# Optimization experiments

Hardware: AMD Instinct MI355X
Metric: run time of the kernel (lower is better)

The kernel has to match this reference:

```python
import jax, jax.numpy as jnp
import numpy as np

N, F, D, K = 4096, 128, 64, 2  # nodes, in_dim, out_dim, hops


def setup_inputs() -> dict:
    key = jax.random.key(0)
    k_x, k_a, k_e, k_w = jax.random.split(key, 4)
    X = jax.random.normal(k_x, (N, F), jnp.float32)
    # K+1 non-negative dense adjacency/distance matrices (stacked list)
    A = jax.random.uniform(k_a, (K + 1, N, N), jnp.float32)
    # Dense(out_dim, use_bias=False) weights, glorot-like scale
    W_emb = jax.random.normal(k_e, (F, D), jnp.float32) / np.sqrt(F)
    W_hops = jax.random.normal(k_w, (K + 1, F, D), jnp.float32) / np.sqrt(F)
    alpha = jnp.float32(0.1)
    return {"X": X, "A": A, "W_emb": W_emb, "W_hops": W_hops, "alpha": alpha}


def reference(X, A, W_emb, W_hops, alpha):
    # learned embeddings E = Dense(X)  -> [N, D]
    E = X @ W_emb
    # shared low-rank update alpha * E @ E^T  -> [N, N]
    low_rank = alpha * (E @ E.T)
    # per-hop kernel projections Dense_k(X)  -> [K+1, N, D]
    XW = jnp.einsum('nf,kfd->knd', X, W_hops)
    out = jnp.zeros((N, D), X.dtype)
    for k in range(A.shape[0]):  # fixed small K+1 hops
        A_hat = A[k] + low_rank                       # [N, N]
        deg = jnp.sum(A_hat, axis=1)                  # row sums
        d = jnp.power(deg, -0.5)                      # D^{-1/2}
        # D^{-1/2} A_hat D^{-1/2} via broadcast scaling (same math as diag matmuls)
        A_norm = d[:, None] * A_hat * d[None, :]
        out = out + A_norm @ XW[k]
    return jax.nn.relu(out)
```

## Files before the change

kernel.cpp:

```cpp
#include <hip/hip_runtime.h>
#include <math.h>

#define N_ 4096
#define F_ 128
#define D_ 64
#define KH_ 3
#define ZS_ 16
#define KC_ (N_ / ZS_)
#define BM_ 256

#define OFF_E      0
#define OFF_XW     (N_*D_)
#define OFF_SE     (OFF_XW + KH_*N_*D_)
#define OFF_T      (OFF_SE + D_)
#define OFF_DVEC   (OFF_T + KH_*D_*D_)
#define OFF_YT     (OFF_DVEC + KH_*N_)
#define OFF_AYP    (OFF_YT + KH_*D_*N_/2)
#define OFF_ABF    (OFF_AYP + ZS_*KH_*N_*D_)

typedef __attribute__((ext_vector_type(8))) short bf16x8;
typedef __attribute__((ext_vector_type(4))) float f32x4;

static __device__ __forceinline__ unsigned short f2bf(float f) {
  union { float f; unsigned u; } v; v.f = f;
  unsigned r = (v.u + 0x7fffu + ((v.u >> 16) & 1u)) >> 16;
  return (unsigned short)r;
}

static __device__ __forceinline__ void gload_lds16(const unsigned short* g,
                                                   unsigned short* l) {
  __builtin_amdgcn_global_load_lds(
      (__attribute__((address_space(1))) unsigned int*)g,
      (__attribute__((address_space(3))) unsigned int*)l, 16, 0, 0);
}

__global__ __launch_bounds__(256) void proj_kernel(
    const float* __restrict__ X, const float* __restrict__ W_emb,
    const float* __restrict__ W_hops, float* __restrict__ ws)
{
  __shared__ __align__(16) float sXT[32][68];
  __shared__ __align__(16) float sW[32][68];
  const int t = threadIdx.x;
  const int m = blockIdx.y;
  const int row0 = blockIdx.x * 64;
  const float* W = (m == 0) ? W_emb : (W_hops + (size_t)(m - 1) * F_ * D_);
  float* out = (m == 0) ? (ws + OFF_E) : (ws + OFF_XW + (size_t)(m - 1) * N_ * D_);
  const int tx = t & 15, ty = t >> 4;
  const int d0 = tx * 4, i0 = ty * 4;
  float acc[4][4] = {};
  for (int fc = 0; fc < F_; fc += 32) {
    {
      int i_l = t >> 3;
      int f_l = (t & 7) * 4;
      for (int r = 0; r < 2; ++r) {
        int i = i_l + r * 32;
        float4 v = *(const float4*)(X + (size_t)(row0 + i) * F_ + fc + f_l);
        sXT[f_l + 0][i] = v.x; sXT[f_l + 1][i] = v.y;
        sXT[f_l + 2][i] = v.z; sXT[f_l + 3][i] = v.w;
      }
      int f2 = t >> 4;
      int d  = (t & 15) * 4;
      for (int r = 0; r < 2; ++r) {
        int f = f2 + r * 16;
        *(float4*)&sW[f][d] = *(const float4*)(W + (size_t)(fc + f) * D_ + d);
      }
    }
    __syncthreads();
#pragma unroll 8
    for (int f = 0; f < 32; ++f) {
      float a[4], b[4];
      *(float4*)a = *(const float4*)&sXT[f][i0];
      *(float4*)b = *(const float4*)&sW[f][d0];
      for (int x = 0; x < 4; ++x)
        for (int y = 0; y < 4; ++y)
          acc[x][y] += a[x] * b[y];
    }
    __syncthreads();
  }
  for (int x = 0; x < 4; ++x)
    *(float4*)(out + (size_t)(row0 + i0 + x) * D_ + d0) = *(float4*)acc[x];
  if (m == 0) {
    float p[4];
    for (int y = 0; y < 4; ++y)
      p[y] = acc[0][y] + acc[1][y] + acc[2][y] + acc[3][y];
    *(float4*)&sXT[ty][d0] = *(float4*)p;
    __syncthreads();
    if (ty < 4) {
      int c = ty * 16 + tx;
      float s = 0.f;
#pragma unroll
      for (int r = 0; r < 16; ++r) s += sXT[r][c];
      atomicAdd(ws + OFF_SE + c, s);
    }
  }
}

__global__ __launch_bounds__(256) void degconv_kernel(
    const float* __restrict__ A, const float* __restrict__ E,
    const float* __restrict__ S, const float* __restrict__ alpha_p,
    float* __restrict__ dvec, unsigned short* __restrict__ Abf)
{
  int lane = threadIdx.x & 63;
  int wave = threadIdx.x >> 6;
  int row = blockIdx.x * 4 + wave;
  int i = row & (N_ - 1);
  const float4* Ar = (const float4*)(A + (size_t)row * N_);
  unsigned short* Br = Abf + (size_t)row * N_;
  float s = 0.f;
#pragma unroll
  for (int it = 0; it < 8; ++it) {
    float4 v0 = Ar[it * 128 + lane * 2 + 0];
    float4 v1 = Ar[it * 128 + lane * 2 + 1];
    s += (v0.x + v0.y) + (v0.z + v0.w) + (v1.x + v1.y) + (v1.z + v1.w);
    union { unsigned short u[8]; uint4 q; } pk;
    pk.u[0] = f2bf(v0.x); pk.u[1] = f2bf(v0.y);
    pk.u[2] = f2bf(v0.z); pk.u[3] = f2bf(v0.w);
    pk.u[4] = f2bf(v1.x); pk.u[5] = f2bf(v1.y);
    pk.u[6] = f2bf(v1.z); pk.u[7] = f2bf(v1.w);
    *(uint4*)(Br + (size_t)it * 512 + lane * 8) = pk.q;
  }
  float alpha = *alpha_p;
  s += alpha * E[(size_t)i * D_ + lane] * S[lane];
#pragma unroll
  for (int off = 32; off > 0; off >>= 1)
    s += __shfl_xor(s, off);
  if (lane == 0) dvec[row] = 1.0f / sqrtf(s);
}

__global__ __launch_bounds__(256) void prep_kernel(float* __restrict__ ws,
                                                   float* __restrict__ T)
{
  const int k = blockIdx.y;
  const float* XWk = ws + OFF_XW + (size_t)k * N_ * D_;
  const float* dk  = ws + OFF_DVEC + (size_t)k * N_;
  int t = threadIdx.x;

  if (blockIdx.x < 64) {
    const int j0 = blockIdx.x * 64;
    unsigned short* Ytk = (unsigned short*)(ws + OFF_YT) + (size_t)k * D_ * N_;
    __shared__ float sT[64][65];
    {
      int j = t >> 2;
      int c0 = (t & 3) * 16;
      float dv = dk[j0 + j];
      for (int r = 0; r < 4; ++r) {
        float4 v = *(const float4*)(XWk + (size_t)(j0 + j) * D_ + c0 + 4 * r);
        sT[c0 + 4 * r + 0][j] = v.x * dv;
        sT[c0 + 4 * r + 1][j] = v.y * dv;
        sT[c0 + 4 * r + 2][j] = v.z * dv;
        sT[c0 + 4 * r + 3][j] = v.w * dv;
      }
    }
    __syncthreads();
    {
      int n = t >> 2;
      int jq = (t & 3) * 16;
      __align__(16) unsigned short buf[16];
#pragma unroll
      for (int i = 0; i < 16; ++i) buf[i] = f2bf(sT[n][jq + i]);
      uint4* dst = (uint4*)(Ytk + (size_t)n * N_ + j0 + jq);
      dst[0] = *(uint4*)&buf[0];
      dst[1] = *(uint4*)&buf[8];
    }
  } else {
    const float* E = ws + OFF_E;
    __shared__ __align__(16) float sE[32][68];
    __shared__ __align__(16) float sY[32][68];
    int tx = t & 15, ty = t >> 4;
    int d0 = tx * 4, c0 = ty * 4;
    float acc[4][4] = {};
    int base0 = (blockIdx.x - 64) * 128;
    for (int sub = 0; sub < 4; ++sub) {
      int base = base0 + sub * 32;
      {
        int i_l = t >> 3;
        int c   = (t & 7) * 4;
        float dv = dk[base + i_l];
        for (int r = 0; r < 2; ++r) {
          int col = c + r * 32;
          *(float4*)&sE[i_l][col] = *(const float4*)(E + (size_t)(base + i_l) * D_ + col);
          float4 y = *(const float4*)(XWk + (size_t)(base + i_l) * D_ + col);
          y.x *= dv; y.y *= dv; y.z *= dv; y.w *= dv;
          *(float4*)&sY[i_l][col] = y;
        }
      }
      __syncthreads();
#pragma unroll 8
      for (int i = 0; i < 32; ++i) {
        float c4[4], y4[4];
        *(float4*)c4 = *(const float4*)&sE[i][c0];
        *(float4*)y4 = *(const float4*)&sY[i][d0];
        for (int a = 0; a < 4; ++a)
          for (int b = 0; b < 4; ++b)
            acc[a][b] += c4[a] * y4[b];
      }
      __syncthreads();
    }
    float* Tk = T + (size_t)k * D_ * D_;
    for (int a = 0; a < 4; ++a)
      for (int b = 0; b < 4; ++b)
        atomicAdd(&Tk[(c0 + a) * D_ + d0 + b], acc[a][b]);
  }
}

__global__ __launch_bounds__(256, 3) void agemm_kernel(
    const float* __restrict__ ws, float* __restrict__ AYp)
{
  const int k = blockIdx.y;
  const int row0 = blockIdx.x * BM_;
  const int kz0 = blockIdx.z * KC_;
  const unsigned short* Ak = (const unsigned short*)(ws + OFF_ABF) + ((size_t)k << 24);
  const unsigned short* Ytk = (const unsigned short*)(ws + OFF_YT) + (size_t)k * D_ * N_;

  __shared__ __align__(16) unsigned short sA[BM_ * 64];
  __shared__ __align__(16) unsigned short sY[64 * 64];

  const int t = threadIdx.x;
  const int lane = t & 63;
  const int w = t >> 6;
  const int m = lane & 15;
  const int q = lane >> 4;
  const int sr = t >> 3;
  const int sc = t & 7;

  f32x4 acc[4][4];
#pragma unroll
  for (int a = 0; a < 4; ++a)
#pragma unroll
    for (int b = 0; b < 4; ++b) acc[a][b] = (f32x4){0.f, 0.f, 0.f, 0.f};

  for (int kt = 0; kt < KC_; kt += 64) {
#pragma unroll
    for (int j = 0; j < 8; ++j) {
      int r = j * 32 + sr;
      gload_lds16(Ak + (size_t)(row0 + r) * N_ + (kz0 + kt) + ((sc ^ (r & 7)) << 3),
                  &sA[j * 2048 + t * 8]);
    }
#pragma unroll
    for (int j = 0; j < 2; ++j) {
      int r = j * 32 + sr;
      gload_lds16(Ytk + (size_t)r * N_ + (kz0 + kt) + ((sc ^ (r & 7)) << 3),
                  &sY[j * 2048 + t * 8]);
    }
    __syncthreads();
#pragma unroll
    for (int s = 0; s < 2; ++s) {
      bf16x8 av[4], bv[4];
#pragma unroll
      for (int mr = 0; mr < 4; ++mr) {
        int row = w * 64 + mr * 16 + m;
        av[mr] = *(const bf16x8*)&sA[row * 64 + (((s * 4 + q) ^ (row & 7)) << 3)];
      }
#pragma unroll
      for (int nt = 0; nt < 4; ++nt) {
        int n = nt * 16 + m;
        bv[nt] = *(const bf16x8*)&sY[n * 64 + (((s * 4 + q) ^ (n & 7)) << 3)];
      }
#pragma unroll
      for (int mr = 0; mr < 4; ++mr)
#pragma unroll
        for (int nt = 0; nt < 4; ++nt)
          acc[mr][nt] = __builtin_amdgcn_mfma_f32_16x16x32_bf16(av[mr], bv[nt],
                                                                acc[mr][nt], 0, 0, 0);
    }
    __syncthreads();
  }
#pragma unroll
  for (int mr = 0; mr < 4; ++mr) {
    float* outp = AYp + (((size_t)blockIdx.z * KH_ + k) * N_ + row0 + w * 64 + mr * 16) * D_;
#pragma unroll
    for (int nt = 0; nt < 4; ++nt)
#pragma unroll
      for (int r = 0; r < 4; ++r)
        outp[(size_t)(q * 4 + r) * D_ + nt * 16 + m] = acc[mr][nt][r];
  }
}

__global__ __launch_bounds__(256) void epilogue_kernel(
    const float* __restrict__ ws, const float* __restrict__ alpha_p,
    float* __restrict__ out)
{
  int g = blockIdx.x * 256 + threadIdx.x;
  int i = g >> 6, d = g & 63;
  const float* E    = ws + OFF_E;
  const float* T    = ws + OFF_T;
  const float* dvec = ws + OFF_DVEC;
  const float* AYp  = ws + OFF_AYP;
  float alpha = *alpha_p;
  float s = 0.f;
  for (int k = 0; k < KH_; ++k) {
    float ay = 0.f;
#pragma unroll
    for (int jc = 0; jc < ZS_; ++jc)
      ay += AYp[(((size_t)jc * KH_ + k) * N_ + i) * D_ + d];
    float lr = 0.f;
    const float* Tk = T + k * D_ * D_;
#pragma unroll 16
    for (int c = 0; c < D_; ++c)
      lr += E[(size_t)i * D_ + c] * Tk[c * D_ + d];
    s += dvec[k * N_ + i] * (ay + alpha * lr);
  }
  out[g] = fmaxf(s, 0.f);
}

extern "C" void kernel_launch(void* const* d_in, const int* in_sizes, int n_in,
                              void* d_out, int out_size, void* d_ws, size_t ws_size,
                              hipStream_t stream) {
  const float* X      = (const float*)d_in[0];
  const float* A      = (const float*)d_in[1];
  const float* W_emb  = (const float*)d_in[2];
  const float* W_hops = (const float*)d_in[3];
  const float* alpha_p= (const float*)d_in[4];
  float* out = (float*)d_out;
  float* ws  = (float*)d_ws;

  hipMemsetAsync(ws + OFF_SE, 0, (D_ + KH_ * D_ * D_) * sizeof(float), stream);

  proj_kernel<<<dim3(N_ / 64, 4), 256, 0, stream>>>(X, W_emb, W_hops, ws);
  degconv_kernel<<<dim3(KH_ * N_ / 4), 256, 0, stream>>>(
      A, ws + OFF_E, ws + OFF_SE, alpha_p, ws + OFF_DVEC,
      (unsigned short*)(ws + OFF_ABF));
  prep_kernel<<<dim3(96, KH_), 256, 0, stream>>>(ws, ws + OFF_T);
  agemm_kernel<<<dim3(N_ / BM_, KH_, ZS_), 256, 0, stream>>>(ws, ws + OFF_AYP);
  epilogue_kernel<<<dim3(N_ * D_ / 256), 256, 0, stream>>>(ws, alpha_p, out);
}
```

Before: 373.0 us.

## Reorder degree pass before projection, defer rsqrt to prep, fold memset

The A row-sum and bf16 conversion kernel no longer depends on the embedding projection, so it now runs first. It stores raw row sums, and the prep kernel adds the alpha*E·S low-rank term and takes the rsqrt. The workspace memset is folded into block 0 of the degree kernel, removing one launch, and the A reads use nontemporal loads to reduce cache pollution. In exchange, prep recomputes the E·S dot products redundantly across its two block types.

```diff
diff --git a/kernel.cpp b/kernel.cpp
--- a/kernel.cpp
+++ b/kernel.cpp
@@ -13,7 +13,8 @@
 #define OFF_XW     (N_*D_)
 #define OFF_SE     (OFF_XW + KH_*N_*D_)
 #define OFF_T      (OFF_SE + D_)
-#define OFF_DVEC   (OFF_T + KH_*D_*D_)
+#define OFF_RS     (OFF_T + KH_*D_*D_)
+#define OFF_DVEC   (OFF_RS + KH_*N_)
 #define OFF_YT     (OFF_DVEC + KH_*N_)
 #define OFF_AYP    (OFF_YT + KH_*D_*N_/2)
 #define OFF_ABF    (OFF_AYP + ZS_*KH_*N_*D_)
@@ -32,6 +33,37 @@
   __builtin_amdgcn_global_load_lds(
       (__attribute__((address_space(1))) unsigned int*)g,
       (__attribute__((address_space(3))) unsigned int*)l, 16, 0, 0);
+}
+
+__global__ __launch_bounds__(256) void degconv_kernel(
+    const float* __restrict__ A, float* __restrict__ ws)
+{
+  if (blockIdx.x == 0) {
+    for (int i = threadIdx.x; i < D_ + KH_ * D_ * D_; i += 256)
+      ws[OFF_SE + i] = 0.f;
+  }
+  int lane = threadIdx.x & 63;
+  int wave = threadIdx.x >> 6;
+  int row = blockIdx.x * 4 + wave;
+  const f32x4* Ar = (const f32x4*)(A + (size_t)row * N_);
+  unsigned short* Br = (unsigned short*)(ws + OFF_ABF) + (size_t)row * N_;
+  float s = 0.f;
+#pragma unroll
+  for (int it = 0; it < 8; ++it) {
+    f32x4 v0 = __builtin_nontemporal_load(Ar + it * 128 + lane * 2 + 0);
+    f32x4 v1 = __builtin_nontemporal_load(Ar + it * 128 + lane * 2 + 1);
+    s += (v0[0] + v0[1]) + (v0[2] + v0[3]) + (v1[0] + v1[1]) + (v1[2] + v1[3]);
+    union { unsigned short u[8]; uint4 q; } pk;
+    pk.u[0] = f2bf(v0[0]); pk.u[1] = f2bf(v0[1]);
+    pk.u[2] = f2bf(v0[2]); pk.u[3] = f2bf(v0[3]);
+    pk.u[4] = f2bf(v1[0]); pk.u[5] = f2bf(v1[1]);
+    pk.u[6] = f2bf(v1[2]); pk.u[7] = f2bf(v1[3]);
+    *(uint4*)(Br + (size_t)it * 512 + lane * 8) = pk.q;
+  }
+#pragma unroll
+  for (int off = 32; off > 0; off >>= 1)
+    s += __shfl_xor(s, off);
+  if (lane == 0) ws[OFF_RS + row] = s;
 }
 
 __global__ __launch_bounds__(256) void proj_kernel(
@@ -95,54 +127,45 @@
   }
 }
 
-__global__ __launch_bounds__(256) void degconv_kernel(
-    const float* __restrict__ A, const float* __restrict__ E,
-    const float* __restrict__ S, const float* __restrict__ alpha_p,
-    float* __restrict__ dvec, unsigned short* __restrict__ Abf)
-{
-  int lane = threadIdx.x & 63;
-  int wave = threadIdx.x >> 6;
-  int row = blockIdx.x * 4 + wave;
-  int i = row & (N_ - 1);
-  const float4* Ar = (const float4*)(A + (size_t)row * N_);
-  unsigned short* Br = Abf + (size_t)row * N_;
-  float s = 0.f;
-#pragma unroll
-  for (int it = 0; it < 8; ++it) {
-    float4 v0 = Ar[it * 128 + lane * 2 + 0];
-    float4 v1 = Ar[it * 128 + lane * 2 + 1];
-    s += (v0.x + v0.y) + (v0.z + v0.w) + (v1.x + v1.y) + (v1.z + v1.w);
-    union { unsigned short u[8]; uint4 q; } pk;
-    pk.u[0] = f2bf(v0.x); pk.u[1] = f2bf(v0.y);
-    pk.u[2] = f2bf(v0.z); pk.u[3] = f2bf(v0.w);
-    pk.u[4] = f2bf(v1.x); pk.u[5] = f2bf(v1.y);
-    pk.u[6] = f2bf(v1.z); pk.u[7] = f2bf(v1.w);
-    *(uint4*)(Br + (size_t)it * 512 + lane * 8) = pk.q;
-  }
-  float alpha = *alpha_p;
-  s += alpha * E[(size_t)i * D_ + lane] * S[lane];
-#pragma unroll
-  for (int off = 32; off > 0; off >>= 1)
-    s += __shfl_xor(s, off);
-  if (lane == 0) dvec[row] = 1.0f / sqrtf(s);
-}
-
 __global__ __launch_bounds__(256) void prep_kernel(float* __restrict__ ws,
-                                                   float* __restrict__ T)
+                                                   const float* __restrict__ alpha_p)
 {
   const int k = blockIdx.y;
   const float* XWk = ws + OFF_XW + (size_t)k * N_ * D_;
-  const float* dk  = ws + OFF_DVEC + (size_t)k * N_;
+  const float* E   = ws + OFF_E;
+  const float* Sv  = ws + OFF_SE;
+  const float* rs  = ws + OFF_RS + (size_t)k * N_;
+  const float alpha = *alpha_p;
   int t = threadIdx.x;
 
   if (blockIdx.x < 64) {
     const int j0 = blockIdx.x * 64;
     unsigned short* Ytk = (unsigned short*)(ws + OFF_YT) + (size_t)k * D_ * N_;
+    __shared__ float sS[64];
+    __shared__ float d_l[64];
+    __shared__ __align__(16) float sEy[64][65];
     __shared__ float sT[64][65];
+    if (t < 64) sS[t] = Sv[t];
     {
       int j = t >> 2;
       int c0 = (t & 3) * 16;
-      float dv = dk[j0 + j];
+      for (int r = 0; r < 4; ++r)
+        *(float4*)&sEy[j][c0 + 4 * r] = *(const float4*)(E + (size_t)(j0 + j) * D_ + c0 + 4 * r);
+    }
+    __syncthreads();
+    if (t < 64) {
+      float dot = 0.f;
+#pragma unroll 16
+      for (int c = 0; c < 64; ++c) dot += sEy[t][c] * sS[c];
+      float dv = 1.0f / sqrtf(rs[j0 + t] + alpha * dot);
+      d_l[t] = dv;
+      ws[OFF_DVEC + (size_t)k * N_ + j0 + t] = dv;
+    }
+    __syncthreads();
+    {
+      int j = t >> 2;
+      int c0 = (t & 3) * 16;
+      float dv = d_l[j];
       for (int r = 0; r < 4; ++r) {
         float4 v = *(const float4*)(XWk + (size_t)(j0 + j) * D_ + c0 + 4 * r);
         sT[c0 + 4 * r + 0][j] = v.x * dv;
@@ -163,19 +186,30 @@
       dst[1] = *(uint4*)&buf[8];
     }
   } else {
-    const float* E = ws + OFF_E;
+    __shared__ float sS2[64];
+    __shared__ float dl2[128];
     __shared__ __align__(16) float sE[32][68];
     __shared__ __align__(16) float sY[32][68];
+    int base0 = (blockIdx.x - 64) * 128;
+    if (t < 64) sS2[t] = Sv[t];
+    __syncthreads();
+    if (t < 128) {
+      int jr = base0 + t;
+      float dot = 0.f;
+#pragma unroll 16
+      for (int c = 0; c < 64; ++c) dot += E[(size_t)jr * D_ + c] * sS2[c];
+      dl2[t] = 1.0f / sqrtf(rs[jr] + alpha * dot);
+    }
+    __syncthreads();
     int tx = t & 15, ty = t >> 4;
     int d0 = tx * 4, c0 = ty * 4;
     float acc[4][4] = {};
-    int base0 = (blockIdx.x - 64) * 128;
     for (int sub = 0; sub < 4; ++sub) {
       int base = base0 + sub * 32;
       {
         int i_l = t >> 3;
         int c   = (t & 7) * 4;
-        float dv = dk[base + i_l];
+        float dv = dl2[sub * 32 + i_l];
         for (int r = 0; r < 2; ++r) {
           int col = c + r * 32;
           *(float4*)&sE[i_l][col] = *(const float4*)(E + (size_t)(base + i_l) * D_ + col);
@@ -196,7 +230,7 @@
       }
       __syncthreads();
     }
-    float* Tk = T + (size_t)k * D_ * D_;
+    float* Tk = ws + OFF_T + (size_t)k * D_ * D_;
     for (int a = 0; a < 4; ++a)
       for (int b = 0; b < 4; ++b)
         atomicAdd(&Tk[(c0 + a) * D_ + d0 + b], acc[a][b]);
@@ -314,13 +348,9 @@
   float* out = (float*)d_out;
   float* ws  = (float*)d_ws;
 
-  hipMemsetAsync(ws + OFF_SE, 0, (D_ + KH_ * D_ * D_) * sizeof(float), stream);
-
+  degconv_kernel<<<dim3(KH_ * N_ / 4), 256, 0, stream>>>(A, ws);
   proj_kernel<<<dim3(N_ / 64, 4), 256, 0, stream>>>(X, W_emb, W_hops, ws);
-  degconv_kernel<<<dim3(KH_ * N_ / 4), 256, 0, stream>>>(
-      A, ws + OFF_E, ws + OFF_SE, alpha_p, ws + OFF_DVEC,
-      (unsigned short*)(ws + OFF_ABF));
-  prep_kernel<<<dim3(96, KH_), 256, 0, stream>>>(ws, ws + OFF_T);
+  prep_kernel<<<dim3(96, KH_), 256, 0, stream>>>(ws, alpha_p);
   agemm_kernel<<<dim3(N_ / BM_, KH_, ZS_), 256, 0, stream>>>(ws, ws + OFF_AYP);
   epilogue_kernel<<<dim3(N_ * D_ / 256), 256, 0, stream>>>(ws, alpha_p, out);
 }
```

Result: faster. 351.0 us (-5.9%).
